# Optimization experiments

Hardware: AMD Instinct MI355X
Metric: run time of the kernel (lower is better)

Reference implementation:

```python
import jax, jax.numpy as jnp
import numpy as np

K = 10
REG = 1e-6


def setup_inputs() -> dict:
    key = jax.random.key(0)
    k1, k2 = jax.random.split(key)
    X = jax.random.normal(k1, (8192, 512), dtype=jnp.float32)
    Z = jax.random.normal(k2, (8192, 64), dtype=jnp.float32)
    return {"X": X, "Z": Z}


def reference(X, Z):
    n, d = X.shape
    # pairwise euclidean distances (torch.cdist): ||xi - xj||
    sq = jnp.sum(X * X, axis=-1)                      # [n]
    D2 = sq[:, None] + sq[None, :] - 2.0 * (X @ X.T)  # [n, n]
    D = jnp.sqrt(jnp.maximum(D2, 0.0))
    # k+1 smallest (self + k neighbors)
    _, knn = jax.lax.top_k(-D, K + 1)                 # [n, k+1]
    neighbors = knn[:, 1:]                            # [n, k]
    # batched local Gram solve for reconstruction weights
    Xj = X[neighbors]                                 # [n, k, d]
    diff = Xj - X[:, None, :]                         # [n, k, d]
    C = jnp.einsum('nkd,nld->nkl', diff, diff)        # [n, k, k]
    C = C + REG * jnp.eye(K, dtype=X.dtype)
    ones = jnp.ones((n, K), dtype=X.dtype)
    w = jnp.linalg.solve(C, ones[..., None])[..., 0]  # [n, k]
    W = w / jnp.sum(w, axis=-1, keepdims=True)
    # weighted reconstruction of latents from neighbor latents
    Z_recon = jnp.einsum('nk,nkd->nd', W, Z[neighbors])
    return jnp.mean((Z_recon - Z) ** 2)
```

## Files before the change

kernel.cpp:

```cpp
#include <hip/hip_runtime.h>
#include <hip/hip_bf16.h>
#include <float.h>
#include <stdint.h>

#define N 8192
#define D 512
#define DZ 64
#define KNN 10
#define REGC 1e-6f
#define KEYBIAS 4096.0f

#define BT 128
#define BK 32
#define NBLK (N / BT)
#define NT (D / BK)

typedef __attribute__((ext_vector_type(8))) short short8v;
typedef __attribute__((ext_vector_type(4))) float f32x4;
typedef __attribute__((ext_vector_type(4))) int int4v;
typedef __attribute__((ext_vector_type(4))) uint uint4v;

#define WAITV0 asm volatile("s_waitcnt vmcnt(0)" ::: "memory")
#define BAR __builtin_amdgcn_s_barrier()

__device__ __forceinline__ void gld16(const ushort* g, ushort* l) {
  __builtin_amdgcn_global_load_lds(
      (const __attribute__((address_space(1))) uint32_t*)g,
      (__attribute__((address_space(3))) uint32_t*)l, 16, 0, 0);
}

__device__ __forceinline__ float b2f(ushort u) {
  return __uint_as_float(((uint)u) << 16);
}

#define INS2(L0, L1, xv)                 \
  do {                                   \
    const uint _x = (xv);                \
    const uint _lo = _x < L0 ? _x : L0;  \
    const uint _hi = _x < L0 ? L0 : _x;  \
    L0 = _lo;                            \
    L1 = _hi < L1 ? _hi : L1;            \
  } while (0)

__global__ __launch_bounds__(64) void prep_kernel(const float* __restrict__ X,
                                                  float* __restrict__ sqb,
                                                  ushort* __restrict__ Xb) {
  const int i = blockIdx.x;
  const int lane = threadIdx.x;
  const float4 v0 = *(const float4*)&X[(size_t)i * D + lane * 8];
  const float4 v1 = *(const float4*)&X[(size_t)i * D + lane * 8 + 4];
  float vv[8] = {v0.x, v0.y, v0.z, v0.w, v1.x, v1.y, v1.z, v1.w};
  ushort h[8];
  float s = 0.f;
#pragma unroll
  for (int j = 0; j < 8; ++j) {
    s = fmaf(vv[j], vv[j], s);
    __hip_bfloat16 b = __float2bfloat16(vv[j]);
    h[j] = *(ushort*)&b;
  }
  *(int4v*)&Xb[(size_t)i * D + lane * 8] = *(int4v*)h;
#pragma unroll
  for (int off = 32; off; off >>= 1) s += __shfl_xor(s, off);
  if (lane == 0) sqb[i] = s + KEYBIAS;
}

__global__ __launch_bounds__(256, 4) void knn_kernel(const ushort* __restrict__ Xb,
                                                     const float* __restrict__ sqb,
                                                     uint* __restrict__ cand) {
  const int bx = blockIdx.x, by = blockIdx.y;
  if (by < bx) return;

  __shared__ ushort As[2][BT][BK];
  __shared__ ushort Bs[2][BT][BK];

  const int i0 = bx * BT;
  const int j0 = by * BT;
  const int tid = threadIdx.x;
  const int lane = tid & 63;
  const int wave = tid >> 6;
  const int wr = wave >> 1, wc = wave & 1;
  const int q = lane >> 4, cr = lane & 15;

  const int srow = tid >> 2, sg = tid & 3;
  const int scsw = (sg ^ ((srow >> 1) & 3)) * 8;
  const size_t aoff0 = (size_t)(i0 + srow) * D + scsw;
  const size_t aoff1 = (size_t)(i0 + 64 + srow) * D + scsw;
  const size_t boff0 = (size_t)(j0 + srow) * D + scsw;
  const size_t boff1 = (size_t)(j0 + 64 + srow) * D + scsw;

  const int fcol = (q ^ ((cr >> 1) & 3)) * 8;

  auto STAGE = [&](int tt) {
    const int bf = tt & 1;
    const int ko = (tt & 15) * BK;
    gld16(Xb + aoff0 + ko, &As[bf][srow][sg * 8]);
    gld16(Xb + aoff1 + ko, &As[bf][64 + srow][sg * 8]);
    gld16(Xb + boff0 + ko, &Bs[bf][srow][sg * 8]);
    gld16(Xb + boff1 + ko, &Bs[bf][64 + srow][sg * 8]);
  };

  f32x4 acc[4][4];
#pragma unroll
  for (int n = 0; n < 4; ++n)
#pragma unroll
    for (int m = 0; m < 4; ++m) acc[n][m] = (f32x4){0.f, 0.f, 0.f, 0.f};

  STAGE(0);

#pragma unroll 1
  for (int t = 0; t < NT; ++t) {
    const int buf = t & 1;
    WAITV0;
    BAR;
    STAGE((t + 1) & (NT - 1));

    const ushort(*Ab)[BK] = As[buf];
    const ushort(*Bb)[BK] = Bs[buf];
    short8v a[4], b[4];
#pragma unroll
    for (int m = 0; m < 4; ++m)
      a[m] = *(const short8v*)&Ab[wr * 64 + m * 16 + cr][fcol];
#pragma unroll
    for (int n = 0; n < 4; ++n)
      b[n] = *(const short8v*)&Bb[wc * 64 + n * 16 + cr][fcol];
    __builtin_amdgcn_s_setprio(1);
#pragma unroll
    for (int n = 0; n < 4; ++n)
#pragma unroll
      for (int m = 0; m < 4; ++m)
        acc[n][m] = __builtin_amdgcn_mfma_f32_16x16x32_bf16(b[n], a[m], acc[n][m], 0, 0, 0);
    __builtin_amdgcn_s_setprio(0);
  }

  float sjv[4][4];
#pragma unroll
  for (int n = 0; n < 4; ++n) {
    const float4 tt = *(const float4*)&sqb[j0 + wc * 64 + n * 16 + q * 4];
    sjv[n][0] = tt.x; sjv[n][1] = tt.y; sjv[n][2] = tt.z; sjv[n][3] = tt.w;
  }
#pragma unroll
  for (int m = 0; m < 4; ++m) {
    uint A0 = 0xFFFFFFFFu, A1 = 0xFFFFFFFFu;
#pragma unroll
    for (int n = 0; n < 4; ++n)
#pragma unroll
      for (int s = 0; s < 4; ++s) {
        const float f = fmaf(-2.f, acc[n][m][s], sjv[n][s]);
        const uint pk = (__float_as_uint(f) & 0xFFFFFF80u) |
                        (uint)(wc * 64 + n * 16 + q * 4 + s);
        INS2(A0, A1, pk);
      }
    uint t0 = __shfl_xor(A0, 16), t1 = __shfl_xor(A1, 16);
    INS2(A0, A1, t0); INS2(A0, A1, t1);
    t0 = __shfl_xor(A0, 32); t1 = __shfl_xor(A1, 32);
    INS2(A0, A1, t0); INS2(A0, A1, t1);
    if (q == 0) {
      uint2 v; v.x = A0; v.y = A1;
      *(uint2*)&cand[(size_t)(i0 + wr * 64 + m * 16 + cr) * 256 + by * 4 + wc * 2] = v;
    }
  }

  if (bx != by) {
    float siv[4];
#pragma unroll
    for (int m = 0; m < 4; ++m) siv[m] = sqb[i0 + wr * 64 + m * 16 + cr];
#pragma unroll
    for (int n = 0; n < 4; ++n)
#pragma unroll
      for (int s = 0; s < 4; ++s) {
        uint B0 = 0xFFFFFFFFu, B1 = 0xFFFFFFFFu;
#pragma unroll
        for (int m = 0; m < 4; ++m) {
          const float f = fmaf(-2.f, acc[n][m][s], siv[m]);
          const uint pk = (__float_as_uint(f) & 0xFFFFFF80u) |
                          (uint)(wr * 64 + m * 16 + cr);
          INS2(B0, B1, pk);
        }
#pragma unroll
        for (int off = 1; off <= 8; off <<= 1) {
          const uint u0 = __shfl_xor(B0, off), u1 = __shfl_xor(B1, off);
          INS2(B0, B1, u0); INS2(B0, B1, u1);
        }
        if ((lane & 15) == 0) {
          uint2 v; v.x = B0; v.y = B1;
          *(uint2*)&cand[(size_t)(j0 + wc * 64 + n * 16 + q * 4 + s) * 256 +
                         bx * 4 + wr * 2] = v;
        }
      }
  }
}

__global__ __launch_bounds__(256) void lle_loss_kernel(
    const ushort* __restrict__ Xb, const float* __restrict__ Z,
    const uint* __restrict__ cand, float* __restrict__ rowsse) {
  const int lane = threadIdx.x & 63;
  const int i = blockIdx.x * 4 + (threadIdx.x >> 6);

  const uint4v pk4 = *(const uint4v*)&cand[(size_t)i * 256 + lane * 4];
  unsigned long long cvm[4];
#pragma unroll
  for (int kk = 0; kk < 4; ++kk) {
    const int g = lane * BT + (int)(pk4[kk] & 0x7Fu);
    const unsigned long long kv =
        ((unsigned long long)(pk4[kk] >> 7) << 13) | (unsigned long long)g;
    cvm[kk] = (g == i) ? ~0ull : kv;
  }

  int nbrj[KNN];
#pragma unroll
  for (int k = 0; k < KNN; ++k) {
    const unsigned long long m01 = cvm[0] < cvm[1] ? cvm[0] : cvm[1];
    const unsigned long long m23 = cvm[2] < cvm[3] ? cvm[2] : cvm[3];
    unsigned long long mn = m01 < m23 ? m01 : m23;
#pragma unroll
    for (int off = 32; off; off >>= 1) {
      const unsigned long long o = __shfl_xor(mn, off);
      mn = o < mn ? o : mn;
    }
    nbrj[k] = (int)(mn & 0x1FFFull);
#pragma unroll
    for (int kk = 0; kk < 4; ++kk)
      cvm[kk] = (cvm[kk] == mn) ? ~0ull : cvm[kk];
  }

  float xi[8];
  {
    const short8v v = *(const short8v*)&Xb[(size_t)i * D + lane * 8];
#pragma unroll
    for (int c = 0; c < 8; ++c) xi[c] = b2f((ushort)v[c]);
  }

  float df[KNN][8];
#pragma unroll
  for (int k = 0; k < KNN; ++k) {
    const int j = nbrj[k];
    const short8v v = *(const short8v*)&Xb[(size_t)j * D + lane * 8];
#pragma unroll
    for (int c = 0; c < 8; ++c) df[k][c] = b2f((ushort)v[c]) - xi[c];
  }

  float C[KNN][KNN];
#pragma unroll
  for (int k = 0; k < KNN; ++k) {
#pragma unroll
    for (int l = 0; l <= k; ++l) {
      float p = 0.f;
#pragma unroll
      for (int c = 0; c < 8; ++c) p = fmaf(df[k][c], df[l][c], p);
#pragma unroll
      for (int off = 32; off; off >>= 1) p += __shfl_xor(p, off);
      C[k][l] = p;
    }
  }

  float dinv[KNN];
#pragma unroll
  for (int j = 0; j < KNN; ++j) {
    float s = C[j][j] + REGC;
#pragma unroll
    for (int t = 0; t < KNN; ++t)
      if (t < j) s -= C[j][t] * C[j][t];
    const float dj = sqrtf(s);
    const float inv = 1.f / dj;
    dinv[j] = inv;
#pragma unroll
    for (int r2 = 0; r2 < KNN; ++r2) {
      if (r2 > j) {
        float s2 = C[r2][j];
#pragma unroll
        for (int t = 0; t < KNN; ++t)
          if (t < j) s2 -= C[r2][t] * C[j][t];
        C[r2][j] = s2 * inv;
      }
    }
  }
  float y[KNN], w[KNN];
#pragma unroll
  for (int r2 = 0; r2 < KNN; ++r2) {
    float s = 1.f;
#pragma unroll
    for (int t = 0; t < KNN; ++t)
      if (t < r2) s -= C[r2][t] * y[t];
    y[r2] = s * dinv[r2];
  }
#pragma unroll
  for (int r2 = KNN - 1; r2 >= 0; --r2) {
    float s2 = y[r2];
#pragma unroll
    for (int t = 0; t < KNN; ++t)
      if (t > r2) s2 -= C[t][r2] * w[t];
    w[r2] = s2 * dinv[r2];
  }
  float ws = 0.f;
#pragma unroll
  for (int k = 0; k < KNN; ++k) ws += w[k];
  const float winv = 1.f / ws;

  float zr = 0.f;
#pragma unroll
  for (int k = 0; k < KNN; ++k)
    zr = fmaf(w[k] * winv, Z[(size_t)nbrj[k] * DZ + lane], zr);
  const float e = zr - Z[(size_t)i * DZ + lane];
  float se = e * e;
#pragma unroll
  for (int off = 32; off; off >>= 1) se += __shfl_xor(se, off);
  if (lane == 0) rowsse[i] = se;
}

__global__ __launch_bounds__(256) void reduce_kernel(const float* __restrict__ rowsse,
                                                     float* __restrict__ out) {
  const int tid = threadIdx.x;
  float s = 0.f;
#pragma unroll
  for (int c = 0; c < N / 256; ++c) s += rowsse[c * 256 + tid];
#pragma unroll
  for (int off = 32; off; off >>= 1) s += __shfl_xor(s, off);
  __shared__ float part[4];
  if ((tid & 63) == 0) part[tid >> 6] = s;
  __syncthreads();
  if (tid == 0)
    out[0] = (part[0] + part[1] + part[2] + part[3]) * (1.f / ((float)N * DZ));
}

extern "C" void kernel_launch(void* const* d_in, const int* in_sizes, int n_in,
                              void* d_out, int out_size, void* d_ws, size_t ws_size,
                              hipStream_t stream) {
  const float* X = (const float*)d_in[0];
  const float* Z = (const float*)d_in[1];
  float* out = (float*)d_out;

  char* ws = (char*)d_ws;
  float* sqb = (float*)ws;
  float* rowsse = (float*)(ws + 32 * 1024);
  ushort* Xb = (ushort*)(ws + 64 * 1024);
  uint* cand = (uint*)(ws + 64 * 1024 + (size_t)N * D * 2);

  prep_kernel<<<N, 64, 0, stream>>>(X, sqb, Xb);
  knn_kernel<<<dim3(NBLK, NBLK), 256, 0, stream>>>(Xb, sqb, cand);
  lle_loss_kernel<<<N / 4, 256, 0, stream>>>(Xb, Z, cand, rowsse);
  reduce_kernel<<<1, 256, 0, stream>>>(rowsse, out);
}
```

Before: 127.0 us.

## Schedule symmetric KNN tiles with circular-offset pairing to balance blocks

Replaces the 64x64 grid, where blocks below the diagonal exit immediately, with a 64x16 grid. Each block processes two (sometimes three) tile pairs chosen by circular offset, so the 2080 upper-triangle tiles are spread evenly over 1024 blocks. The A tile for a row block is reused across consecutive pairs, and the top-2 candidate extraction runs after each pair within a single pipelined loop. This removes wasted empty-block launches and tail imbalance, but adds per-pair epilogue work inside the main loop and an uneven extra pair for half of the final group.

```diff
diff --git a/kernel.cpp b/kernel.cpp
--- a/kernel.cpp
+++ b/kernel.cpp
@@ -13,7 +13,6 @@
 #define BT 128
 #define BK 32
 #define NBLK (N / BT)
-#define NT (D / BK)
 
 typedef __attribute__((ext_vector_type(8))) short short8v;
 typedef __attribute__((ext_vector_type(4))) float f32x4;
@@ -67,14 +66,14 @@
 __global__ __launch_bounds__(256, 4) void knn_kernel(const ushort* __restrict__ Xb,
                                                      const float* __restrict__ sqb,
                                                      uint* __restrict__ cand) {
-  const int bx = blockIdx.x, by = blockIdx.y;
-  if (by < bx) return;
-
   __shared__ ushort As[2][BT][BK];
   __shared__ ushort Bs[2][BT][BK];
 
-  const int i0 = bx * BT;
-  const int j0 = by * BT;
+  const int x = blockIdx.x;
+  const int g = blockIdx.y;
+  const int npairs = (g == 15 && x < 32) ? 3 : 2;
+  const int nsteps = npairs * 16;
+
   const int tid = threadIdx.x;
   const int lane = tid & 63;
   const int wave = tid >> 6;
@@ -83,20 +82,26 @@
 
   const int srow = tid >> 2, sg = tid & 3;
   const int scsw = (sg ^ ((srow >> 1) & 3)) * 8;
-  const size_t aoff0 = (size_t)(i0 + srow) * D + scsw;
-  const size_t aoff1 = (size_t)(i0 + 64 + srow) * D + scsw;
-  const size_t boff0 = (size_t)(j0 + srow) * D + scsw;
-  const size_t boff1 = (size_t)(j0 + 64 + srow) * D + scsw;
+  const size_t aoff0 = (size_t)(x * BT + srow) * D + scsw;
+  const size_t aoff1 = aoff0 + (size_t)64 * D;
+  const size_t soff = (size_t)srow * D + scsw;
 
   const int fcol = (q ^ ((cr >> 1) & 3)) * 8;
 
-  auto STAGE = [&](int tt) {
-    const int bf = tt & 1;
-    const int ko = (tt & 15) * BK;
+  auto tbOf = [&](int p) {
+    const int d = (p == 2) ? 32 : (2 * g + p);
+    return (x + d) & 63;
+  };
+
+  auto STAGE = [&](int s) {
+    const int p = s >> 4;
+    const int bf = s & 1;
+    const int ko = (s & 15) * BK;
+    const size_t boff = ((size_t)tbOf(p) * BT) * D + soff;
     gld16(Xb + aoff0 + ko, &As[bf][srow][sg * 8]);
     gld16(Xb + aoff1 + ko, &As[bf][64 + srow][sg * 8]);
-    gld16(Xb + boff0 + ko, &Bs[bf][srow][sg * 8]);
-    gld16(Xb + boff1 + ko, &Bs[bf][64 + srow][sg * 8]);
+    gld16(Xb + boff + ko, &Bs[bf][srow][sg * 8]);
+    gld16(Xb + boff + (size_t)64 * D + ko, &Bs[bf][64 + srow][sg * 8]);
   };
 
   f32x4 acc[4][4];
@@ -108,11 +113,12 @@
   STAGE(0);
 
 #pragma unroll 1
-  for (int t = 0; t < NT; ++t) {
+  for (int t = 0; t < nsteps; ++t) {
     const int buf = t & 1;
     WAITV0;
     BAR;
-    STAGE((t + 1) & (NT - 1));
+    const int nx = t + 1;
+    STAGE(nx >= nsteps ? 0 : nx);
 
     const ushort(*Ab)[BK] = As[buf];
     const ushort(*Bb)[BK] = Bs[buf];
@@ -130,63 +136,74 @@
       for (int m = 0; m < 4; ++m)
         acc[n][m] = __builtin_amdgcn_mfma_f32_16x16x32_bf16(b[n], a[m], acc[n][m], 0, 0, 0);
     __builtin_amdgcn_s_setprio(0);
-  }
-
-  float sjv[4][4];
-#pragma unroll
-  for (int n = 0; n < 4; ++n) {
-    const float4 tt = *(const float4*)&sqb[j0 + wc * 64 + n * 16 + q * 4];
-    sjv[n][0] = tt.x; sjv[n][1] = tt.y; sjv[n][2] = tt.z; sjv[n][3] = tt.w;
-  }
-#pragma unroll
-  for (int m = 0; m < 4; ++m) {
-    uint A0 = 0xFFFFFFFFu, A1 = 0xFFFFFFFFu;
-#pragma unroll
-    for (int n = 0; n < 4; ++n)
-#pragma unroll
-      for (int s = 0; s < 4; ++s) {
-        const float f = fmaf(-2.f, acc[n][m][s], sjv[n][s]);
-        const uint pk = (__float_as_uint(f) & 0xFFFFFF80u) |
-                        (uint)(wc * 64 + n * 16 + q * 4 + s);
-        INS2(A0, A1, pk);
+
+    if ((t & 15) == 15) {
+      const int tb = tbOf(t >> 4);
+      const int j0 = tb * BT;
+
+      float sjv[4][4];
+#pragma unroll
+      for (int n = 0; n < 4; ++n) {
+        const float4 tt = *(const float4*)&sqb[j0 + wc * 64 + n * 16 + q * 4];
+        sjv[n][0] = tt.x; sjv[n][1] = tt.y; sjv[n][2] = tt.z; sjv[n][3] = tt.w;
       }
-    uint t0 = __shfl_xor(A0, 16), t1 = __shfl_xor(A1, 16);
-    INS2(A0, A1, t0); INS2(A0, A1, t1);
-    t0 = __shfl_xor(A0, 32); t1 = __shfl_xor(A1, 32);
-    INS2(A0, A1, t0); INS2(A0, A1, t1);
-    if (q == 0) {
-      uint2 v; v.x = A0; v.y = A1;
-      *(uint2*)&cand[(size_t)(i0 + wr * 64 + m * 16 + cr) * 256 + by * 4 + wc * 2] = v;
-    }
-  }
-
-  if (bx != by) {
-    float siv[4];
-#pragma unroll
-    for (int m = 0; m < 4; ++m) siv[m] = sqb[i0 + wr * 64 + m * 16 + cr];
-#pragma unroll
-    for (int n = 0; n < 4; ++n)
-#pragma unroll
-      for (int s = 0; s < 4; ++s) {
-        uint B0 = 0xFFFFFFFFu, B1 = 0xFFFFFFFFu;
-#pragma unroll
-        for (int m = 0; m < 4; ++m) {
-          const float f = fmaf(-2.f, acc[n][m][s], siv[m]);
-          const uint pk = (__float_as_uint(f) & 0xFFFFFF80u) |
-                          (uint)(wr * 64 + m * 16 + cr);
-          INS2(B0, B1, pk);
-        }
-#pragma unroll
-        for (int off = 1; off <= 8; off <<= 1) {
-          const uint u0 = __shfl_xor(B0, off), u1 = __shfl_xor(B1, off);
-          INS2(B0, B1, u0); INS2(B0, B1, u1);
-        }
-        if ((lane & 15) == 0) {
-          uint2 v; v.x = B0; v.y = B1;
-          *(uint2*)&cand[(size_t)(j0 + wc * 64 + n * 16 + q * 4 + s) * 256 +
-                         bx * 4 + wr * 2] = v;
+#pragma unroll
+      for (int m = 0; m < 4; ++m) {
+        uint A0 = 0xFFFFFFFFu, A1 = 0xFFFFFFFFu;
+#pragma unroll
+        for (int n = 0; n < 4; ++n)
+#pragma unroll
+          for (int s = 0; s < 4; ++s) {
+            const float f = fmaf(-2.f, acc[n][m][s], sjv[n][s]);
+            const uint pk = (__float_as_uint(f) & 0xFFFFFF80u) |
+                            (uint)(wc * 64 + n * 16 + q * 4 + s);
+            INS2(A0, A1, pk);
+          }
+        uint t0 = __shfl_xor(A0, 16), t1 = __shfl_xor(A1, 16);
+        INS2(A0, A1, t0); INS2(A0, A1, t1);
+        t0 = __shfl_xor(A0, 32); t1 = __shfl_xor(A1, 32);
+        INS2(A0, A1, t0); INS2(A0, A1, t1);
+        if (q == 0) {
+          uint2 v; v.x = A0; v.y = A1;
+          *(uint2*)&cand[(size_t)(x * BT + wr * 64 + m * 16 + cr) * 256 +
+                         tb * 4 + wc * 2] = v;
         }
       }
+
+      if (tb != x) {
+        float siv[4];
+#pragma unroll
+        for (int m = 0; m < 4; ++m) siv[m] = sqb[x * BT + wr * 64 + m * 16 + cr];
+#pragma unroll
+        for (int n = 0; n < 4; ++n)
+#pragma unroll
+          for (int s = 0; s < 4; ++s) {
+            uint B0 = 0xFFFFFFFFu, B1 = 0xFFFFFFFFu;
+#pragma unroll
+            for (int m = 0; m < 4; ++m) {
+              const float f = fmaf(-2.f, acc[n][m][s], siv[m]);
+              const uint pk = (__float_as_uint(f) & 0xFFFFFF80u) |
+                              (uint)(wr * 64 + m * 16 + cr);
+              INS2(B0, B1, pk);
+            }
+#pragma unroll
+            for (int off = 1; off <= 8; off <<= 1) {
+              const uint u0 = __shfl_xor(B0, off), u1 = __shfl_xor(B1, off);
+              INS2(B0, B1, u0); INS2(B0, B1, u1);
+            }
+            if ((lane & 15) == 0) {
+              uint2 v; v.x = B0; v.y = B1;
+              *(uint2*)&cand[(size_t)(j0 + wc * 64 + n * 16 + q * 4 + s) * 256 +
+                             x * 4 + wr * 2] = v;
+            }
+          }
+      }
+
+#pragma unroll
+      for (int n = 0; n < 4; ++n)
+#pragma unroll
+        for (int m = 0; m < 4; ++m) acc[n][m] = (f32x4){0.f, 0.f, 0.f, 0.f};
+    }
   }
 }
 
@@ -336,7 +353,7 @@
   uint* cand = (uint*)(ws + 64 * 1024 + (size_t)N * D * 2);
 
   prep_kernel<<<N, 64, 0, stream>>>(X, sqb, Xb);
-  knn_kernel<<<dim3(NBLK, NBLK), 256, 0, stream>>>(Xb, sqb, cand);
+  knn_kernel<<<dim3(NBLK, 16), 256, 0, stream>>>(Xb, sqb, cand);
   lle_loss_kernel<<<N / 4, 256, 0, stream>>>(Xb, Z, cand, rowsse);
   reduce_kernel<<<1, 256, 0, stream>>>(rowsse, out);
 }
```

New measurement: 138.5 us. 1.09x slower.
